# Kernel optimization log

Hardware: AMD Instinct MI355X
Metric: run time of the kernel (lower is better)

The kernel has to match this reference:

```python
import jax, jax.numpy as jnp
import numpy as np

B, N, C, K = 16, 1024, 192, 9
H = 4 * C  # hidden of second MLP pair


def _gelu(x):
    return jax.nn.gelu(x, approximate=False)  # torch nn.GELU default is exact erf


def _mlp(x, w1, b1, w2, b2):
    # TwoLayerNN: Linear -> GELU -> Linear
    return _gelu(x @ w1.T + b1) @ w2.T + b2


def _linear_init(key, out_d, in_d):
    k1, k2 = jax.random.split(key)
    s = 1.0 / np.sqrt(in_d)
    w = jax.random.uniform(k1, (out_d, in_d), minval=-s, maxval=s, dtype=jnp.float32)
    b = jax.random.uniform(k2, (out_d,), minval=-s, maxval=s, dtype=jnp.float32)
    return w, b


def setup_inputs() -> dict:
    key = jax.random.key(0)
    ks = jax.random.split(key, 10)
    x = jax.random.normal(ks[0], (B, N, C), dtype=jnp.float32)
    il1_w1, il1_b1 = _linear_init(ks[1], C, C)
    il1_w2, il1_b2 = _linear_init(ks[2], C, C)
    ol1_w1, ol1_b1 = _linear_init(ks[3], C, C)
    ol1_w2, ol1_b2 = _linear_init(ks[4], C, C)
    il2_w1, il2_b1 = _linear_init(ks[5], H, C)
    il2_w2, il2_b2 = _linear_init(ks[6], C, H)
    ol2_w1, ol2_b1 = _linear_init(ks[7], H, C)
    ol2_w2, ol2_b2 = _linear_init(ks[8], C, H)
    fc_w, fc_b = _linear_init(ks[9], C, 2 * C)  # Conv1d(2C, C, 1) == Linear(2C->C)
    return dict(x=x,
                il1_w1=il1_w1, il1_b1=il1_b1, il1_w2=il1_w2, il1_b2=il1_b2,
                fc_w=fc_w, fc_b=fc_b,
                ol1_w1=ol1_w1, ol1_b1=ol1_b1, ol1_w2=ol1_w2, ol1_b2=ol1_b2,
                il2_w1=il2_w1, il2_b1=il2_b1, il2_w2=il2_w2, il2_b2=il2_b2,
                ol2_w1=ol2_w1, ol2_b1=ol2_b1, ol2_w2=ol2_w2, ol2_b2=ol2_b2)


def reference(x, il1_w1, il1_b1, il1_w2, il1_b2, fc_w, fc_b,
              ol1_w1, ol1_b1, ol1_w2, ol1_b2,
              il2_w1, il2_b1, il2_w2, il2_b2,
              ol2_w1, ol2_b1, ol2_w2, ol2_b2):
    Bx, Nx, Cx = x.shape
    # 1) dense similarity + KNN graph (indices only; no grad path through sim)
    sim = jnp.einsum('bnc,bmc->bnm', x, x)                       # [B,N,N]
    _, graph = jax.lax.top_k(sim, K)                             # [B,N,K] int32
    shortcut = x
    # 2) node transform then gather-max aggregation
    h = _mlp(x.reshape(Bx * Nx, Cx), il1_w1, il1_b1, il1_w2, il1_b2).reshape(Bx, Nx, Cx)
    nb = jnp.take_along_axis(h[:, None, :, :], graph[:, :, :, None], axis=2)  # [B,N,K,C]
    agg = jnp.max(nb - h[:, :, None, :], axis=2)                 # [B,N,C]
    # 3) stack along new last dim then flatten -> interleaved channels [x_c0,agg_c0,x_c1,...]
    cat = jnp.stack([h, agg], axis=-1).reshape(Bx, Nx, 2 * Cx)   # [B,N,2C]
    h = cat @ fc_w.T + fc_b                                      # Conv1d k=1 == Linear
    h = _mlp(_gelu(h).reshape(Bx * Nx, Cx), ol1_w1, ol1_b1, ol1_w2, ol1_b2).reshape(Bx, Nx, Cx)
    x1 = h + shortcut
    # 4) FFN block (two TwoLayerNNs with external GELU between them)
    f = _mlp(x1.reshape(Bx * Nx, Cx), il2_w1, il2_b1, il2_w2, il2_b2)
    f = _mlp(_gelu(f), ol2_w1, ol2_b1, ol2_w2, ol2_b2).reshape(Bx, Nx, Cx)
    return f + x1
```

## Files before the change

kernel.cpp:

```cpp
#include <hip/hip_runtime.h>
#include <hip/hip_bf16.h>
#include <math.h>

#define DEVINL __device__ __forceinline__

typedef __attribute__((ext_vector_type(4))) float f32x4;
typedef __attribute__((ext_vector_type(8))) short s16x8;

DEVINL unsigned short f2bf(float f) {
  union { float f; unsigned u; } v; v.f = f;
  unsigned r = v.u + 0x7FFFu + ((v.u >> 16) & 1u);
  return (unsigned short)(r >> 16);
}
DEVINL float bf2f(unsigned short s) {
  union { unsigned u; float f; } v; v.u = ((unsigned)s) << 16;
  return v.f;
}
DEVINL float gelu_exact(float x) {
  return 0.5f * x * (1.0f + erff(x * 0.70710678118654752f));
}

__global__ __launch_bounds__(256) void conv_kernel(const float* __restrict__ x,
                                                   unsigned short* __restrict__ xh,
                                                   unsigned short* __restrict__ xl) {
  int i = blockIdx.x * 256 + threadIdx.x;
  float4 v = ((const float4*)x)[i];
  float f[4] = {v.x, v.y, v.z, v.w};
  unsigned short h[4], l[4];
#pragma unroll
  for (int j = 0; j < 4; ++j) {
    h[j] = f2bf(f[j]);
    l[j] = f2bf(f[j] - bf2f(h[j]));
  }
  uint2 uh, ul;
  uh.x = (unsigned)h[0] | ((unsigned)h[1] << 16);
  uh.y = (unsigned)h[2] | ((unsigned)h[3] << 16);
  ul.x = (unsigned)l[0] | ((unsigned)l[1] << 16);
  ul.y = (unsigned)l[2] | ((unsigned)l[3] << 16);
  ((uint2*)xh)[i] = uh;
  ((uint2*)xl)[i] = ul;
}

__global__ __launch_bounds__(512)
#if __has_attribute(amdgpu_waves_per_eu)
__attribute__((amdgpu_waves_per_eu(2, 2)))
#endif
void simtopk_kernel(const unsigned short* __restrict__ xh,
                    const unsigned short* __restrict__ xl,
                    int* __restrict__ graph) {
  const int tid  = threadIdx.x;
  const int lane = tid & 63;
  const int w    = tid >> 6;
  const int rb   = blockIdx.x;
  const int b    = blockIdx.y;
  const int wm   = w >> 1, wn = w & 1;

  extern __shared__ char smem[];
  unsigned short* colsH = (unsigned short*)smem;
  unsigned short* colsL = (unsigned short*)(smem + 49152);
  float* simt = (float*)(smem + 98304);
  float* mv   = (float*)smem;
  int*   mix  = (int*)(smem + 18432);

  const unsigned short* xhb = xh + (size_t)b * (1024 * 192);
  const unsigned short* xlb = xl + (size_t)b * (1024 * 192);

  s16x8 ah[6], al[6];
#pragma unroll
  for (int ks = 0; ks < 6; ++ks) {
    int r = rb * 64 + wm * 16 + (lane & 15);
    size_t off = (size_t)r * 192 + ks * 32 + (lane >> 4) * 8;
    ah[ks] = *(const s16x8*)(xhb + off);
    al[ks] = *(const s16x8*)(xlb + off);
  }

  auto stage = [&](int buf, int ct) {
#pragma unroll
    for (int i = 0; i < 3; ++i) {
      int c = tid + i * 512;
      int row = c / 24, cc = c - row * 24;
      size_t goff = (size_t)(ct * 64 + row) * 192 + (size_t)((cc ^ (row & 7)) * 8);
      unsigned short* dstH = colsH + buf * 12288 + (w * 64 + i * 512) * 8;
      unsigned short* dstL = colsL + buf * 12288 + (w * 64 + i * 512) * 8;
      __builtin_amdgcn_global_load_lds((const __attribute__((address_space(1))) void*)(xhb + goff),
                                       (__attribute__((address_space(3))) void*)dstH, 16, 0, 0);
      __builtin_amdgcn_global_load_lds((const __attribute__((address_space(1))) void*)(xlb + goff),
                                       (__attribute__((address_space(3))) void*)dstL, 16, 0, 0);
    }
  };

  float tv[9]; int tix[9];
#pragma unroll
  for (int k = 0; k < 9; ++k) { tv[k] = -3.0e38f; tix[k] = 1 << 30; }

  stage(0, 0);
  __syncthreads();

  for (int ct = 0; ct < 16; ++ct) {
    const int cur = ct & 1;
    if (ct < 15) stage(cur ^ 1, ct + 1);

    f32x4 a0[2], a1[2], a2[2];
#pragma unroll
    for (int n2 = 0; n2 < 2; ++n2) { a0[n2] = 0; a1[n2] = 0; a2[n2] = 0; }

#pragma unroll
    for (int ks = 0; ks < 6; ++ks) {
      const int chk = ks * 4 + (lane >> 4);
#pragma unroll
      for (int n2 = 0; n2 < 2; ++n2) {
        int r = wn * 32 + n2 * 16 + (lane & 15);
        int si = cur * 12288 + r * 192 + ((chk ^ (r & 7)) * 8);
        s16x8 bh = *(const s16x8*)&colsH[si];
        s16x8 bl = *(const s16x8*)&colsL[si];
        a0[n2] = __builtin_amdgcn_mfma_f32_16x16x32_bf16(ah[ks], bh, a0[n2], 0, 0, 0);
        a1[n2] = __builtin_amdgcn_mfma_f32_16x16x32_bf16(ah[ks], bl, a1[n2], 0, 0, 0);
        a2[n2] = __builtin_amdgcn_mfma_f32_16x16x32_bf16(al[ks], bh, a2[n2], 0, 0, 0);
      }
    }

#pragma unroll
    for (int n2 = 0; n2 < 2; ++n2)
#pragma unroll
      for (int r = 0; r < 4; ++r) {
        int rr = wm * 16 + (lane >> 4) * 4 + r;
        int cc = wn * 32 + n2 * 16 + (lane & 15);
        simt[rr * 65 + cc] = a0[n2][r] + a1[n2][r] + a2[n2][r];
      }
    __syncthreads();

    {
      int r = tid >> 3, q = tid & 7;
#pragma unroll
      for (int j = 0; j < 8; ++j) {
        float v = simt[r * 65 + q * 8 + j];
        int   c = ct * 64 + q * 8 + j;
        if (v > tv[8]) {
          tv[8] = v; tix[8] = c;
#pragma unroll
          for (int s = 8; s > 0; --s) {
            if (tv[s] > tv[s - 1]) {
              float fv = tv[s]; tv[s] = tv[s - 1]; tv[s - 1] = fv;
              int   fi = tix[s]; tix[s] = tix[s - 1]; tix[s - 1] = fi;
            }
          }
        }
      }
    }
    __syncthreads();
  }

#pragma unroll
  for (int k = 0; k < 9; ++k) { mv[tid * 9 + k] = tv[k]; mix[tid * 9 + k] = tix[k]; }
  __syncthreads();
  if (tid < 64) {
    float fv[9]; int fi[9];
#pragma unroll
    for (int k = 0; k < 9; ++k) { fv[k] = -3.0e38f; fi[k] = 1 << 30; }
    for (int t = 0; t < 8; ++t) {
      int base = (tid * 8 + t) * 9;
#pragma unroll
      for (int k = 0; k < 9; ++k) {
        float v = mv[base + k]; int c = mix[base + k];
        bool better = (v > fv[8]) || (v == fv[8] && c < fi[8]);
        if (better) {
          fv[8] = v; fi[8] = c;
#pragma unroll
          for (int s = 8; s > 0; --s) {
            bool up = (fv[s] > fv[s - 1]) || (fv[s] == fv[s - 1] && fi[s] < fi[s - 1]);
            if (up) {
              float a = fv[s]; fv[s] = fv[s - 1]; fv[s - 1] = a;
              int  ii = fi[s]; fi[s] = fi[s - 1]; fi[s - 1] = ii;
            }
          }
        }
      }
    }
    int* gout = graph + ((size_t)b * 1024 + rb * 64 + tid) * 9;
#pragma unroll
    for (int k = 0; k < 9; ++k) gout[k] = fi[k];
  }
}

__global__ __launch_bounds__(256) void agg_kernel(const unsigned short* __restrict__ h,
                                                  const int* __restrict__ graph,
                                                  unsigned short* __restrict__ cat) {
  int gid  = blockIdx.x * 4 + (threadIdx.x >> 6);
  int lane = threadIdx.x & 63;
  int b = gid >> 10;
  int n = gid & 1023;
  const unsigned short* hb = h + (size_t)b * (1024 * 192);
  const int* g = graph + (size_t)gid * 9;
  float hn[3];
#pragma unroll
  for (int j = 0; j < 3; ++j) hn[j] = bf2f(hb[(size_t)n * 192 + lane + j * 64]);
  float ag[3] = {-3.0e38f, -3.0e38f, -3.0e38f};
  for (int k = 0; k < 9; ++k) {
    int idx = g[k];
#pragma unroll
    for (int j = 0; j < 3; ++j) {
      float v = bf2f(hb[(size_t)idx * 192 + lane + j * 64]) - hn[j];
      ag[j] = fmaxf(ag[j], v);
    }
  }
  unsigned* crow = (unsigned*)cat + (size_t)gid * 192;
#pragma unroll
  for (int j = 0; j < 3; ++j) {
    int c = lane + j * 64;
    crow[c] = (unsigned)f2bf(hn[j]) | ((unsigned)f2bf(ag[j]) << 16);
  }
}

template <bool GELU_, bool RESID>
__global__ __launch_bounds__(256) void gemm_kernel(const unsigned short* __restrict__ A,
                                                   const float* __restrict__ W,
                                                   const float* __restrict__ bias,
                                                   const float* __restrict__ resid,
                                                   unsigned short* __restrict__ outb,
                                                   float* __restrict__ outf,
                                                   int N, int K) {
  __shared__ unsigned short As[2][128 * 64];
  __shared__ unsigned short Ws[2][64 * 64];

  const int tid  = threadIdx.x;
  const int lane = tid & 63;
  const int w    = tid >> 6;
  const int m0   = blockIdx.x * 128;
  const int n0   = blockIdx.y * 64;

  auto stageA = [&](int buf, int kt) {
    const unsigned short* gA = A + (size_t)m0 * K + kt * 64;
#pragma unroll
    for (int i = 0; i < 4; ++i) {
      int chunk = w * 4 + i;
      const unsigned short* src = gA + (size_t)(chunk * 8 + (lane >> 3)) * K + (lane & 7) * 8;
      unsigned short* dst = &As[buf][chunk * 512];
      __builtin_amdgcn_global_load_lds((const __attribute__((address_space(1))) void*)src,
                                       (__attribute__((address_space(3))) void*)dst, 16, 0, 0);
    }
  };
  auto stageW = [&](int buf, int kt) {
#pragma unroll
    for (int i = 0; i < 4; ++i) {
      int idx = tid + i * 256;
      int n = idx >> 4, kq = idx & 15;
      float4 v = *(const float4*)(W + (size_t)(n0 + n) * K + kt * 64 + kq * 4);
      uint2 u;
      u.x = (unsigned)f2bf(v.x) | ((unsigned)f2bf(v.y) << 16);
      u.y = (unsigned)f2bf(v.z) | ((unsigned)f2bf(v.w) << 16);
      *(uint2*)&Ws[buf][n * 64 + kq * 4] = u;
    }
  };

  stageA(0, 0);
  stageW(0, 0);
  __syncthreads();

  const int wm = w >> 1, wn = w & 1;
  f32x4 acc[4][2];
#pragma unroll
  for (int a = 0; a < 4; ++a)
#pragma unroll
    for (int c = 0; c < 2; ++c) acc[a][c] = 0;

  const int nk = K >> 6;
  for (int kt = 0; kt < nk; ++kt) {
    const int cur = kt & 1;
    if (kt + 1 < nk) { stageA(cur ^ 1, kt + 1); stageW(cur ^ 1, kt + 1); }
#pragma unroll
    for (int ks = 0; ks < 2; ++ks) {
      const int ko = ks * 32 + (lane >> 4) * 8;
      s16x8 af[4], bfr[2];
#pragma unroll
      for (int m2 = 0; m2 < 4; ++m2)
        af[m2] = *(const s16x8*)&As[cur][(wm * 64 + m2 * 16 + (lane & 15)) * 64 + ko];
#pragma unroll
      for (int n2 = 0; n2 < 2; ++n2)
        bfr[n2] = *(const s16x8*)&Ws[cur][(wn * 32 + n2 * 16 + (lane & 15)) * 64 + ko];
#pragma unroll
      for (int m2 = 0; m2 < 4; ++m2)
#pragma unroll
        for (int n2 = 0; n2 < 2; ++n2)
          acc[m2][n2] = __builtin_amdgcn_mfma_f32_16x16x32_bf16(af[m2], bfr[n2], acc[m2][n2], 0, 0, 0);
    }
    __syncthreads();
  }

#pragma unroll
  for (int m2 = 0; m2 < 4; ++m2)
#pragma unroll
    for (int n2 = 0; n2 < 2; ++n2)
#pragma unroll
      for (int r = 0; r < 4; ++r) {
        int row = m0 + wm * 64 + m2 * 16 + (lane >> 4) * 4 + r;
        int col = n0 + wn * 32 + n2 * 16 + (lane & 15);
        float v = acc[m2][n2][r] + bias[col];
        if (GELU_) v = gelu_exact(v);
        if (RESID) v += resid[(size_t)row * N + col];
        size_t o = (size_t)row * N + col;
        if (outb) outb[o] = f2bf(v);
        if (outf) outf[o] = v;
      }
}

extern "C" void kernel_launch(void* const* d_in, const int* in_sizes, int n_in,
                              void* d_out, int out_size, void* d_ws, size_t ws_size,
                              hipStream_t stream) {
  (void)in_sizes; (void)n_in; (void)out_size; (void)ws_size;
  const float* x      = (const float*)d_in[0];
  const float* il1_w1 = (const float*)d_in[1];
  const float* il1_b1 = (const float*)d_in[2];
  const float* il1_w2 = (const float*)d_in[3];
  const float* il1_b2 = (const float*)d_in[4];
  const float* fc_w   = (const float*)d_in[5];
  const float* fc_b   = (const float*)d_in[6];
  const float* ol1_w1 = (const float*)d_in[7];
  const float* ol1_b1 = (const float*)d_in[8];
  const float* ol1_w2 = (const float*)d_in[9];
  const float* ol1_b2 = (const float*)d_in[10];
  const float* il2_w1 = (const float*)d_in[11];
  const float* il2_b1 = (const float*)d_in[12];
  const float* il2_w2 = (const float*)d_in[13];
  const float* il2_b2 = (const float*)d_in[14];
  const float* ol2_w1 = (const float*)d_in[15];
  const float* ol2_b1 = (const float*)d_in[16];
  const float* ol2_w2 = (const float*)d_in[17];
  const float* ol2_b2 = (const float*)d_in[18];

  char* ws = (char*)d_ws;
  const size_t SZ = 16384ull * 192 * 2;
  unsigned short* xbf  = (unsigned short*)(ws);
  unsigned short* t13  = (unsigned short*)(ws + SZ);
  unsigned short* hbuf = (unsigned short*)(ws + 2 * SZ);
  unsigned short* t2   = (unsigned short*)(ws + 3 * SZ);
  unsigned short* x1b  = (unsigned short*)(ws + 4 * SZ);
  unsigned short* catg = (unsigned short*)(ws + 5 * SZ);
  float*          x1f  = (float*)(ws + 7 * SZ);
  unsigned short* uv   = (unsigned short*)(ws + 9 * SZ);
  unsigned short* xlo  = uv;
  int*            graph = (int*)(ws + 13 * SZ);

  hipFuncSetAttribute((const void*)simtopk_kernel,
                      hipFuncAttributeMaxDynamicSharedMemorySize, 114944);

  conv_kernel<<<3072, 256, 0, stream>>>(x, xbf, xlo);
  simtopk_kernel<<<dim3(16, 16), 512, 114944, stream>>>(xbf, xlo, graph);
  gemm_kernel<true,  false><<<dim3(128, 3), 256, 0, stream>>>(xbf, il1_w1, il1_b1, nullptr, t13, nullptr, 192, 192);
  gemm_kernel<false, false><<<dim3(128, 3), 256, 0, stream>>>(t13, il1_w2, il1_b2, nullptr, hbuf, nullptr, 192, 192);
  agg_kernel<<<4096, 256, 0, stream>>>(hbuf, graph, catg);
  gemm_kernel<true,  false><<<dim3(128, 3), 256, 0, stream>>>(catg, fc_w, fc_b, nullptr, t2, nullptr, 192, 384);
  gemm_kernel<true,  false><<<dim3(128, 3), 256, 0, stream>>>(t2, ol1_w1, ol1_b1, nullptr, t13, nullptr, 192, 192);
  gemm_kernel<false, true ><<<dim3(128, 3), 256, 0, stream>>>(t13, ol1_w2, ol1_b2, x, x1b, x1f, 192, 192);
  gemm_kernel<true,  false><<<dim3(128, 12), 256, 0, stream>>>(x1b, il2_w1, il2_b1, nullptr, uv, nullptr, 768, 192);
  gemm_kernel<true,  false><<<dim3(128, 3), 256, 0, stream>>>(uv, il2_w2, il2_b2, nullptr, catg, nullptr, 192, 768);
  gemm_kernel<true,  false><<<dim3(128, 12), 256, 0, stream>>>(catg, ol2_w1, ol2_b1, nullptr, uv, nullptr, 768, 192);
  gemm_kernel<false, true ><<<dim3(128, 3), 256, 0, stream>>>(uv, ol2_w2, ol2_b2, x1f, nullptr, (float*)d_out, 192, 768);
}
```

Measured before the change: 297.0 us.

## Halve simtopk row tile to double grid and drop LDS double buffering

The similarity/top-k kernel now processes 32 rows per block instead of 64, which doubles the grid to 512 blocks. The 8 waves are rearranged as 2x4 over a 32x64 tile. Column staging becomes single-buffered and is issued after the sim tile is written, which halves shared memory and raises the waves-per-EU hint so more blocks can be resident. The final merge becomes a two-level reduction (16 partial lists per row, merged 4 then 4). In exchange, each block re-stages all columns with half the reuse, and the load for the next tile is exposed instead of overlapped with compute.

```diff
diff --git a/kernel.cpp b/kernel.cpp
--- a/kernel.cpp
+++ b/kernel.cpp
@@ -43,7 +43,7 @@
 
 __global__ __launch_bounds__(512)
 #if __has_attribute(amdgpu_waves_per_eu)
-__attribute__((amdgpu_waves_per_eu(2, 2)))
+__attribute__((amdgpu_waves_per_eu(4)))
 #endif
 void simtopk_kernel(const unsigned short* __restrict__ xh,
                     const unsigned short* __restrict__ xl,
@@ -53,14 +53,16 @@
   const int w    = tid >> 6;
   const int rb   = blockIdx.x;
   const int b    = blockIdx.y;
-  const int wm   = w >> 1, wn = w & 1;
+  const int wm   = w >> 2, wn = w & 3;
 
   extern __shared__ char smem[];
   unsigned short* colsH = (unsigned short*)smem;
-  unsigned short* colsL = (unsigned short*)(smem + 49152);
-  float* simt = (float*)(smem + 98304);
-  float* mv   = (float*)smem;
-  int*   mix  = (int*)(smem + 18432);
+  unsigned short* colsL = (unsigned short*)(smem + 24576);
+  float* simt = (float*)(smem + 49152);
+  float* Lv = (float*)smem;
+  int*   Li = (int*)(smem + 18432);
+  float* Mv = (float*)(smem + 36864);
+  int*   Mi = (int*)(smem + 41472);
 
   const unsigned short* xhb = xh + (size_t)b * (1024 * 192);
   const unsigned short* xlb = xl + (size_t)b * (1024 * 192);
@@ -68,20 +70,20 @@
   s16x8 ah[6], al[6];
 #pragma unroll
   for (int ks = 0; ks < 6; ++ks) {
-    int r = rb * 64 + wm * 16 + (lane & 15);
+    int r = rb * 32 + wm * 16 + (lane & 15);
     size_t off = (size_t)r * 192 + ks * 32 + (lane >> 4) * 8;
     ah[ks] = *(const s16x8*)(xhb + off);
     al[ks] = *(const s16x8*)(xlb + off);
   }
 
-  auto stage = [&](int buf, int ct) {
+  auto stage = [&](int ct) {
 #pragma unroll
     for (int i = 0; i < 3; ++i) {
       int c = tid + i * 512;
       int row = c / 24, cc = c - row * 24;
       size_t goff = (size_t)(ct * 64 + row) * 192 + (size_t)((cc ^ (row & 7)) * 8);
-      unsigned short* dstH = colsH + buf * 12288 + (w * 64 + i * 512) * 8;
-      unsigned short* dstL = colsL + buf * 12288 + (w * 64 + i * 512) * 8;
+      unsigned short* dstH = colsH + (size_t)c * 8;
+      unsigned short* dstL = colsL + (size_t)c * 8;
       __builtin_amdgcn_global_load_lds((const __attribute__((address_space(1))) void*)(xhb + goff),
                                        (__attribute__((address_space(3))) void*)dstH, 16, 0, 0);
       __builtin_amdgcn_global_load_lds((const __attribute__((address_space(1))) void*)(xlb + goff),
@@ -93,48 +95,40 @@
 #pragma unroll
   for (int k = 0; k < 9; ++k) { tv[k] = -3.0e38f; tix[k] = 1 << 30; }
 
-  stage(0, 0);
+  stage(0);
   __syncthreads();
 
   for (int ct = 0; ct < 16; ++ct) {
-    const int cur = ct & 1;
-    if (ct < 15) stage(cur ^ 1, ct + 1);
-
-    f32x4 a0[2], a1[2], a2[2];
-#pragma unroll
-    for (int n2 = 0; n2 < 2; ++n2) { a0[n2] = 0; a1[n2] = 0; a2[n2] = 0; }
+    f32x4 a0 = 0, a1 = 0, a2 = 0;
 
 #pragma unroll
     for (int ks = 0; ks < 6; ++ks) {
       const int chk = ks * 4 + (lane >> 4);
-#pragma unroll
-      for (int n2 = 0; n2 < 2; ++n2) {
-        int r = wn * 32 + n2 * 16 + (lane & 15);
-        int si = cur * 12288 + r * 192 + ((chk ^ (r & 7)) * 8);
-        s16x8 bh = *(const s16x8*)&colsH[si];
-        s16x8 bl = *(const s16x8*)&colsL[si];
-        a0[n2] = __builtin_amdgcn_mfma_f32_16x16x32_bf16(ah[ks], bh, a0[n2], 0, 0, 0);
-        a1[n2] = __builtin_amdgcn_mfma_f32_16x16x32_bf16(ah[ks], bl, a1[n2], 0, 0, 0);
-        a2[n2] = __builtin_amdgcn_mfma_f32_16x16x32_bf16(al[ks], bh, a2[n2], 0, 0, 0);
-      }
-    }
-
-#pragma unroll
-    for (int n2 = 0; n2 < 2; ++n2)
-#pragma unroll
-      for (int r = 0; r < 4; ++r) {
-        int rr = wm * 16 + (lane >> 4) * 4 + r;
-        int cc = wn * 32 + n2 * 16 + (lane & 15);
-        simt[rr * 65 + cc] = a0[n2][r] + a1[n2][r] + a2[n2][r];
-      }
+      const int rc  = wn * 16 + (lane & 15);
+      const int si  = rc * 192 + ((chk ^ (rc & 7)) * 8);
+      s16x8 bh = *(const s16x8*)&colsH[si];
+      s16x8 bl = *(const s16x8*)&colsL[si];
+      a0 = __builtin_amdgcn_mfma_f32_16x16x32_bf16(ah[ks], bh, a0, 0, 0, 0);
+      a1 = __builtin_amdgcn_mfma_f32_16x16x32_bf16(ah[ks], bl, a1, 0, 0, 0);
+      a2 = __builtin_amdgcn_mfma_f32_16x16x32_bf16(al[ks], bh, a2, 0, 0, 0);
+    }
+
+#pragma unroll
+    for (int r = 0; r < 4; ++r) {
+      int rr = wm * 16 + (lane >> 4) * 4 + r;
+      int cc = wn * 16 + (lane & 15);
+      simt[rr * 65 + cc] = a0[r] + a1[r] + a2[r];
+    }
     __syncthreads();
 
+    if (ct < 15) stage(ct + 1);
+
     {
-      int r = tid >> 3, q = tid & 7;
-#pragma unroll
-      for (int j = 0; j < 8; ++j) {
-        float v = simt[r * 65 + q * 8 + j];
-        int   c = ct * 64 + q * 8 + j;
+      int r = tid >> 4, q = tid & 15;
+#pragma unroll
+      for (int j = 0; j < 4; ++j) {
+        float v = simt[r * 65 + q * 4 + j];
+        int   c = ct * 64 + q * 4 + j;
         if (v > tv[8]) {
           tv[8] = v; tix[8] = c;
 #pragma unroll
@@ -151,17 +145,19 @@
   }
 
 #pragma unroll
-  for (int k = 0; k < 9; ++k) { mv[tid * 9 + k] = tv[k]; mix[tid * 9 + k] = tix[k]; }
+  for (int k = 0; k < 9; ++k) { Lv[tid * 9 + k] = tv[k]; Li[tid * 9 + k] = tix[k]; }
   __syncthreads();
-  if (tid < 64) {
+
+  if (tid < 128) {
+    int r = tid >> 2, p = tid & 3;
     float fv[9]; int fi[9];
 #pragma unroll
     for (int k = 0; k < 9; ++k) { fv[k] = -3.0e38f; fi[k] = 1 << 30; }
-    for (int t = 0; t < 8; ++t) {
-      int base = (tid * 8 + t) * 9;
+    for (int s4 = 0; s4 < 4; ++s4) {
+      int base = (r * 16 + p * 4 + s4) * 9;
 #pragma unroll
       for (int k = 0; k < 9; ++k) {
-        float v = mv[base + k]; int c = mix[base + k];
+        float v = Lv[base + k]; int c = Li[base + k];
         bool better = (v > fv[8]) || (v == fv[8] && c < fi[8]);
         if (better) {
           fv[8] = v; fi[8] = c;
@@ -176,7 +172,35 @@
         }
       }
     }
-    int* gout = graph + ((size_t)b * 1024 + rb * 64 + tid) * 9;
+#pragma unroll
+    for (int k = 0; k < 9; ++k) { Mv[tid * 9 + k] = fv[k]; Mi[tid * 9 + k] = fi[k]; }
+  }
+  __syncthreads();
+
+  if (tid < 32) {
+    float fv[9]; int fi[9];
+#pragma unroll
+    for (int k = 0; k < 9; ++k) { fv[k] = -3.0e38f; fi[k] = 1 << 30; }
+    for (int p = 0; p < 4; ++p) {
+      int base = (tid * 4 + p) * 9;
+#pragma unroll
+      for (int k = 0; k < 9; ++k) {
+        float v = Mv[base + k]; int c = Mi[base + k];
+        bool better = (v > fv[8]) || (v == fv[8] && c < fi[8]);
+        if (better) {
+          fv[8] = v; fi[8] = c;
+#pragma unroll
+          for (int s = 8; s > 0; --s) {
+            bool up = (fv[s] > fv[s - 1]) || (fv[s] == fv[s - 1] && fi[s] < fi[s - 1]);
+            if (up) {
+              float a = fv[s]; fv[s] = fv[s - 1]; fv[s - 1] = a;
+              int  ii = fi[s]; fi[s] = fi[s - 1]; fi[s - 1] = ii;
+            }
+          }
+        }
+      }
+    }
+    int* gout = graph + ((size_t)b * 1024 + rb * 32 + tid) * 9;
 #pragma unroll
     for (int k = 0; k < 9; ++k) gout[k] = fi[k];
   }
@@ -341,10 +365,10 @@
   int*            graph = (int*)(ws + 13 * SZ);
 
   hipFuncSetAttribute((const void*)simtopk_kernel,
-                      hipFuncAttributeMaxDynamicSharedMemorySize, 114944);
+                      hipFuncAttributeMaxDynamicSharedMemorySize, 57472);
 
   conv_kernel<<<3072, 256, 0, stream>>>(x, xbf, xlo);
-  simtopk_kernel<<<dim3(16, 16), 512, 114944, stream>>>(xbf, xlo, graph);
+  simtopk_kernel<<<dim3(32, 16), 512, 57472, stream>>>(xbf, xlo, graph);
   gemm_kernel<true,  false><<<dim3(128, 3), 256, 0, stream>>>(xbf, il1_w1, il1_b1, nullptr, t13, nullptr, 192, 192);
   gemm_kernel<false, false><<<dim3(128, 3), 256, 0, stream>>>(t13, il1_w2, il1_b2, nullptr, hbuf, nullptr, 192, 192);
   agg_kernel<<<4096, 256, 0, stream>>>(hbuf, graph, catg);
```

Result: faster. 266.6 us (-10.2%).
